# Kernel optimization log

Measured on AMD Instinct MI355X. Metric: run time of the kernel, lower is better.

The kernel has to match this reference:

```python
import jax, jax.numpy as jnp
import numpy as np

B = 32768
NUM_DENSE = 13
PAD_DENSE = 16  # 13 padded up to multiple of 8
T = 26          # number of categorical tables
V = 100000      # cardinality per table
E = 128         # embedding_dim
BOTTOM_DIMS = [512, 256, 128]
TOP_DIMS = [1024, 1024, 512, 256, 1]
N_FEAT = T + 1  # 27 feature vectors entering interaction
PAIR = N_FEAT * (N_FEAT - 1) // 2  # 351
TOP_IN = PAIR + E   # 479
TOP_PAD = 480       # padded to multiple of 8


def _glorot(key, fan_in, fan_out):
    s = np.sqrt(2.0 / (fan_in + fan_out))
    return jax.random.normal(key, (fan_in, fan_out), jnp.float32) * s


def setup_inputs() -> dict:
    key = jax.random.key(0)
    ks = jax.random.split(key, 32)
    inp = {
        "numerical": jax.random.normal(ks[0], (B, NUM_DENSE), jnp.float32),
        "cat_features": jax.random.randint(ks[1], (B, T), 0, V, jnp.int32),
        "emb_tables": jax.random.normal(ks[2], (T, V, E), jnp.float32) * 0.01,
    }
    # bottom MLP: 16 -> 512 -> 256 -> 128 (all relu)
    d_in = PAD_DENSE
    for i, d in enumerate(BOTTOM_DIMS):
        inp[f"bw{i}"] = _glorot(ks[3 + 2 * i], d_in, d)
        inp[f"bb{i}"] = jax.random.normal(ks[4 + 2 * i], (d,), jnp.float32) * np.sqrt(1.0 / d)
        d_in = d
    # top MLP: 480 -> 1024 -> 1024 -> 512 -> 256 -> 1 (relu except last)
    d_in = TOP_PAD
    for i, d in enumerate(TOP_DIMS):
        inp[f"tw{i}"] = _glorot(ks[12 + 2 * i], d_in, d)
        inp[f"tb{i}"] = jax.random.normal(ks[13 + 2 * i], (d,), jnp.float32) * np.sqrt(1.0 / d)
        d_in = d
    return inp


def reference(numerical, cat_features, emb_tables,
              bw0, bb0, bw1, bb1, bw2, bb2,
              tw0, tb0, tw1, tb1, tw2, tb2, tw3, tb3, tw4, tb4):
    b = numerical.shape[0]
    # --- bottom MLP (dense features padded with zeros to 16) ---
    x = jnp.pad(numerical, ((0, 0), (0, PAD_DENSE - NUM_DENSE)))
    for w, bias in ((bw0, bb0), (bw1, bb1), (bw2, bb2)):
        x = jax.nn.relu(x @ w + bias)
    bottom_out = x  # [B, E]
    # --- multi-table embedding gather: emb_tables[t][cat[:, t]] ---
    emb_out = jax.vmap(lambda tab, idx: tab[idx], in_axes=(0, 1), out_axes=1)(
        emb_tables, cat_features)  # [B, T, E]
    # --- dot interaction ---
    feats = jnp.concatenate([bottom_out[:, None, :], emb_out], axis=1)  # [B, 27, E]
    Z = jnp.einsum('bnd,bmd->bnm', feats, feats)  # [B, 27, 27]
    iu, ju = jnp.triu_indices(N_FEAT, k=1)
    pair = Z[:, iu, ju]  # [B, 351]
    x = jnp.concatenate(
        [bottom_out, pair, jnp.zeros((b, TOP_PAD - TOP_IN), feats.dtype)], axis=1)  # [B, 480]
    # --- top MLP (relu except last layer) ---
    tops = ((tw0, tb0), (tw1, tb1), (tw2, tb2), (tw3, tb3), (tw4, tb4))
    for i, (w, bias) in enumerate(tops):
        x = x @ w + bias
        if i < len(tops) - 1:
            x = jax.nn.relu(x)
    return x  # [B, 1] logits
```

## Files before the change

### kernel.cpp

```cpp
#include <hip/hip_runtime.h>

typedef __bf16 bf16;
typedef __bf16 bf16x4 __attribute__((ext_vector_type(4)));
typedef __bf16 bf16x8 __attribute__((ext_vector_type(8)));
typedef float f32x4 __attribute__((ext_vector_type(4)));

#define B_SZ 32768
#define T_CAT 26
#define V_SZ 100000
#define E_SZ 128

__device__ __forceinline__ void gload_lds16(const void* g, void* l) {
    __builtin_amdgcn_global_load_lds(
        (const __attribute__((address_space(1))) void*)g,
        (__attribute__((address_space(3))) void*)l, 16, 0, 0);
}

struct CJob { const float* W; bf16* Wt; int K, N, Kp, blk0; };
struct CJobs { CJob j[7]; };

__global__ __launch_bounds__(256) void convw_all(CJobs js) {
    const int b = blockIdx.x;
    int ji = 0;
#pragma unroll
    for (int k = 1; k < 7; ++k)
        if (b >= js.j[k].blk0) ji = k;
    const CJob J = js.j[ji];
    const int idx = (b - J.blk0) * 256 + threadIdx.x;
    if (idx >= J.Kp * J.N) return;
    const int k = idx / J.N;
    const int n = idx - k * J.N;
    const float v = (k < J.K) ? J.W[(long)k * J.N + n] : 0.0f;
    J.Wt[(long)n * J.Kp + k] = (bf16)v;
}

__global__ __launch_bounds__(256) void make_xpad(const float* __restrict__ num,
                                                 bf16* __restrict__ xp) {
    const int idx = blockIdx.x * 256 + threadIdx.x;
    const int b = idx >> 6, c = idx & 63;
    xp[idx] = (bf16)((c < 13) ? num[(long)b * 13 + c] : 0.0f);
}

template <int RELU>
__global__ __launch_bounds__(256) void gemm_bt(const bf16* __restrict__ A,
                                               const bf16* __restrict__ Bt,
                                               const float* __restrict__ bias,
                                               bf16* __restrict__ C,
                                               int M, int N, int K) {
    __shared__ __align__(16) bf16 As[128 * 64];
    __shared__ __align__(16) bf16 Bs[128 * 64];
    const int t = threadIdx.x;
    const int lane = t & 63;
    const int w = t >> 6;
    const int wm = w >> 1, wn = w & 1;
    const long row0 = (long)blockIdx.y * 128;
    const long col0 = (long)blockIdx.x * 128;

    const int srow = t >> 3;
    const int scol = (t & 7) * 8;
    const bf16* Ag = A + (row0 + srow) * (long)K + scol;
    const bf16* Bg = Bt + (col0 + srow) * (long)K + scol;
    bf16* AsB = &As[w * 512];
    bf16* BsB = &Bs[w * 512];

    f32x4 acc[4][4] = {};

    for (int k0 = 0; k0 < K; k0 += 64) {
#pragma unroll
        for (int q = 0; q < 4; ++q) {
            gload_lds16(Ag + (long)q * 32 * K + k0, AsB + q * 2048);
            gload_lds16(Bg + (long)q * 32 * K + k0, BsB + q * 2048);
        }
        __syncthreads();
#pragma unroll
        for (int s = 0; s < 2; ++s) {
            bf16x8 af[4], bv[4];
#pragma unroll
            for (int i = 0; i < 4; ++i)
                af[i] = *(const bf16x8*)&As[(wm * 64 + i * 16 + (lane & 15)) * 64 +
                                            s * 32 + (lane >> 4) * 8];
#pragma unroll
            for (int j = 0; j < 4; ++j)
                bv[j] = *(const bf16x8*)&Bs[(wn * 64 + j * 16 + (lane & 15)) * 64 +
                                            s * 32 + (lane >> 4) * 8];
#pragma unroll
            for (int i = 0; i < 4; ++i)
#pragma unroll
                for (int j = 0; j < 4; ++j)
                    acc[i][j] = __builtin_amdgcn_mfma_f32_16x16x32_bf16(
                        af[i], bv[j], acc[i][j], 0, 0, 0);
        }
        __syncthreads();
    }

    const int r4 = (lane >> 4) * 4;
    const int cn = lane & 15;
#pragma unroll
    for (int j = 0; j < 4; ++j) {
        const long col = col0 + wn * 64 + j * 16 + cn;
        const float bj = bias[col];
#pragma unroll
        for (int i = 0; i < 4; ++i) {
#pragma unroll
            for (int r = 0; r < 4; ++r) {
                const long row = row0 + wm * 64 + i * 16 + r4 + r;
                float v = acc[i][j][r] + bj;
                if (RELU) v = v > 0.0f ? v : 0.0f;
                C[row * (long)N + col] = (bf16)v;
            }
        }
    }
}

template <int RELU>
__global__ __launch_bounds__(512, 2) void gemm256(const bf16* __restrict__ A,
                                                  const bf16* __restrict__ Bt,
                                                  const float* __restrict__ bias,
                                                  bf16* __restrict__ C,
                                                  int M, int N, int K, int nbx) {
    __shared__ __align__(16) bf16 lds[4 * 2 * 8192];
    const int t = threadIdx.x;
    const int lane = t & 63;
    const int w = t >> 6;
    const int wm = w >> 2, wn = w & 3;

    const int nwg = gridDim.x;
    const int qch = nwg >> 3;
    const int swz = ((int)blockIdx.x & 7) * qch + ((int)blockIdx.x >> 3);
    const int bx = swz % nbx, by = swz / nbx;
    const long row0 = (long)by * 256;
    const long col0 = (long)bx * 256;

    const int NT = K >> 5;

    const int lr = lane >> 2;
    const int dslot = lane & 3;
    const int lrow0 = (w * 2 + 0) * 16 + lr;
    const int lrow1 = (w * 2 + 1) * 16 + lr;
    const int sl0 = dslot ^ ((lrow0 >> 1) & 3);
    const int sl1 = dslot ^ ((lrow1 >> 1) & 3);
    const bf16* Ag0 = A + (row0 + lrow0) * (long)K + sl0 * 8;
    const bf16* Ag1 = A + (row0 + lrow1) * (long)K + sl1 * 8;
    const bf16* Bg0 = Bt + (col0 + lrow0) * (long)K + sl0 * 8;
    const bf16* Bg1 = Bt + (col0 + lrow1) * (long)K + sl1 * 8;
    const int ldsRow0 = (w * 2 + 0) * 512;
    const int ldsRow1 = (w * 2 + 1) * 512;

#define STAGE_A(buf, kt)                                                   \
    do {                                                                   \
        const int _k0 = (kt) << 5;                                         \
        gload_lds16(Ag0 + _k0, &lds[((buf) * 2 + 0) * 8192 + ldsRow0]);    \
        gload_lds16(Ag1 + _k0, &lds[((buf) * 2 + 0) * 8192 + ldsRow1]);    \
    } while (0)
#define STAGE_B(buf, kt)                                                   \
    do {                                                                   \
        const int _k0 = (kt) << 5;                                         \
        gload_lds16(Bg0 + _k0, &lds[((buf) * 2 + 1) * 8192 + ldsRow0]);    \
        gload_lds16(Bg1 + _k0, &lds[((buf) * 2 + 1) * 8192 + ldsRow1]);    \
    } while (0)

    const int cm = lane & 15;
    const int kc = lane >> 4;
    int aoff[8], boff[4];
#pragma unroll
    for (int i = 0; i < 8; ++i) {
        const int r = wm * 128 + i * 16 + cm;
        aoff[i] = r * 32 + (kc ^ ((r >> 1) & 3)) * 8;
    }
#pragma unroll
    for (int j = 0; j < 4; ++j) {
        const int n = wn * 64 + j * 16 + cm;
        boff[j] = n * 32 + (kc ^ ((n >> 1) & 3)) * 8;
    }

    f32x4 acc[8][4] = {};

    STAGE_A(0, 0); STAGE_B(0, 0);
    STAGE_A(1, 1); STAGE_B(1, 1);
    STAGE_A(2, 2); STAGE_B(2, 2);

    for (int tt = 0; tt < NT; ++tt) {
        const int rem = NT - 1 - tt;
        const int sb = (tt + 3) & 3;
        const int sk = tt + 3;

        if (rem >= 2)      asm volatile("s_waitcnt vmcnt(8)" ::: "memory");
        else if (rem == 1) asm volatile("s_waitcnt vmcnt(4)" ::: "memory");
        else               asm volatile("s_waitcnt vmcnt(0)" ::: "memory");
        __builtin_amdgcn_s_barrier();

        const bf16* Ab = &lds[((tt & 3) * 2 + 0) * 8192];
        const bf16* Bb = &lds[((tt & 3) * 2 + 1) * 8192];

        bf16x8 bfr[4], af[4];
#pragma unroll
        for (int j = 0; j < 4; ++j) bfr[j] = *(const bf16x8*)&Bb[boff[j]];
#pragma unroll
        for (int i = 0; i < 4; ++i) af[i] = *(const bf16x8*)&Ab[aoff[i]];
        if (rem >= 3) STAGE_A(sb, sk);
        __builtin_amdgcn_s_barrier();
        __builtin_amdgcn_s_setprio(1);
#pragma unroll
        for (int i = 0; i < 4; ++i)
#pragma unroll
            for (int j = 0; j < 4; ++j)
                acc[i][j] = __builtin_amdgcn_mfma_f32_16x16x32_bf16(
                    af[i], bfr[j], acc[i][j], 0, 0, 0);
        __builtin_amdgcn_s_setprio(0);

        bf16x8 af2[4];
#pragma unroll
        for (int i = 0; i < 4; ++i) af2[i] = *(const bf16x8*)&Ab[aoff[4 + i]];
        if (rem >= 3) STAGE_B(sb, sk);
        __builtin_amdgcn_s_barrier();
        __builtin_amdgcn_s_setprio(1);
#pragma unroll
        for (int i = 0; i < 4; ++i)
#pragma unroll
            for (int j = 0; j < 4; ++j)
                acc[4 + i][j] = __builtin_amdgcn_mfma_f32_16x16x32_bf16(
                    af2[i], bfr[j], acc[4 + i][j], 0, 0, 0);
        __builtin_amdgcn_s_setprio(0);
    }
#undef STAGE_A
#undef STAGE_B

    const int r4 = kc * 4;
#pragma unroll
    for (int j = 0; j < 4; ++j) {
        const long col = col0 + wn * 64 + j * 16 + cm;
        const float bj = bias[col];
#pragma unroll
        for (int i = 0; i < 8; ++i) {
#pragma unroll
            for (int r = 0; r < 4; ++r) {
                const long row = row0 + wm * 128 + i * 16 + r4 + r;
                float v = acc[i][j][r] + bj;
                if (RELU) v = v > 0.0f ? v : 0.0f;
                C[row * (long)N + col] = (bf16)v;
            }
        }
    }
}

__global__ __launch_bounds__(256) void interact_k(const float* __restrict__ emb,
                                                  const int* __restrict__ cat,
                                                  const bf16* __restrict__ bottom,
                                                  bf16* __restrict__ top_in) {
    __shared__ __align__(16) bf16 feats[4][32 * 128];
    __shared__ float gram[4][32 * 32];
    __shared__ __align__(16) bf16 rowbuf[4][512];
    const int t = threadIdx.x;
    const int lane = t & 63;
    const int w = t >> 6;
    const long s = (long)blockIdx.x * 4 + w;

    if (lane < 16)
        ((bf16x8*)&feats[w][0])[lane] = ((const bf16x8*)(bottom + s * 128))[lane];

    const int half = lane >> 5;
    const int le = lane & 31;
#pragma unroll
    for (int it = 0; it < 13; ++it) {
        const int r = 1 + it * 2 + half;
        const int tab = r - 1;
        const int idx = cat[s * T_CAT + tab];
        const float4 v =
            *(const float4*)(emb + ((long)tab * V_SZ + idx) * E_SZ + le * 4);
        bf16x4 o;
        o[0] = (bf16)v.x; o[1] = (bf16)v.y; o[2] = (bf16)v.z; o[3] = (bf16)v.w;
        *(bf16x4*)&feats[w][r * 128 + le * 4] = o;
    }
    __syncthreads();

    bf16x8 f[2][4];
#pragma unroll
    for (int i = 0; i < 2; ++i)
#pragma unroll
        for (int ks = 0; ks < 4; ++ks)
            f[i][ks] = *(const bf16x8*)&feats[w][(i * 16 + (lane & 15)) * 128 +
                                                 ks * 32 + (lane >> 4) * 8];

    f32x4 a00 = {}, a01 = {}, a11 = {};
#pragma unroll
    for (int ks = 0; ks < 4; ++ks) {
        a00 = __builtin_amdgcn_mfma_f32_16x16x32_bf16(f[0][ks], f[0][ks], a00, 0, 0, 0);
        a01 = __builtin_amdgcn_mfma_f32_16x16x32_bf16(f[0][ks], f[1][ks], a01, 0, 0, 0);
        a11 = __builtin_amdgcn_mfma_f32_16x16x32_bf16(f[1][ks], f[1][ks], a11, 0, 0, 0);
    }

    const int r4 = (lane >> 4) * 4;
    const int cn = lane & 15;
#pragma unroll
    for (int r = 0; r < 4; ++r) {
        gram[w][(r4 + r) * 32 + cn]           = a00[r];
        gram[w][(r4 + r) * 32 + 16 + cn]      = a01[r];
        gram[w][(16 + r4 + r) * 32 + 16 + cn] = a11[r];
    }
    __syncthreads();

    if (lane < 16)
        ((bf16x8*)&rowbuf[w][0])[lane] = ((const bf16x8*)&feats[w][0])[lane];
    for (int p = lane; p < 351; p += 64) {
        int i = 0, b = 0;
        while (b + (26 - i) <= p) { b += 26 - i; ++i; }
        const int j = p - b + i + 1;
        rowbuf[w][128 + p] = (bf16)gram[w][i * 32 + j];
    }
    if (lane >= 31) rowbuf[w][448 + lane] = (bf16)0.0f;
    __syncthreads();

    *(bf16x8*)(top_in + s * 512 + lane * 8) = *(const bf16x8*)&rowbuf[w][lane * 8];
}

__global__ __launch_bounds__(256) void gemv_final(const bf16* __restrict__ A,
                                                  const float* __restrict__ w4,
                                                  const float* __restrict__ b4,
                                                  float* __restrict__ out) {
    const int t = threadIdx.x;
    const int lane = t & 63;
    const int w = t >> 6;
    const long m = (long)blockIdx.x * 4 + w;
    const bf16x4 v = *(const bf16x4*)(A + m * 256 + lane * 4);
    const float4 wv = *(const float4*)(w4 + lane * 4);
    float sum = (float)v[0] * wv.x + (float)v[1] * wv.y + (float)v[2] * wv.z +
                (float)v[3] * wv.w;
#pragma unroll
    for (int off = 32; off > 0; off >>= 1) sum += __shfl_down(sum, off);
    if (lane == 0) out[m] = sum + b4[0];
}

extern "C" void kernel_launch(void* const* d_in, const int* in_sizes, int n_in,
                              void* d_out, int out_size, void* d_ws, size_t ws_size,
                              hipStream_t stream) {
    const float* numerical = (const float*)d_in[0];
    const int*   cat       = (const int*)d_in[1];
    const float* emb       = (const float*)d_in[2];
    const float* bw0 = (const float*)d_in[3];
    const float* bb0 = (const float*)d_in[4];
    const float* bw1 = (const float*)d_in[5];
    const float* bb1 = (const float*)d_in[6];
    const float* bw2 = (const float*)d_in[7];
    const float* bb2 = (const float*)d_in[8];
    const float* tw0 = (const float*)d_in[9];
    const float* tb0 = (const float*)d_in[10];
    const float* tw1 = (const float*)d_in[11];
    const float* tb1 = (const float*)d_in[12];
    const float* tw2 = (const float*)d_in[13];
    const float* tb2 = (const float*)d_in[14];
    const float* tw3 = (const float*)d_in[15];
    const float* tb3 = (const float*)d_in[16];
    const float* tw4 = (const float*)d_in[17];
    const float* tb4 = (const float*)d_in[18];
    float* out = (float*)d_out;

    char* ws = (char*)d_ws;
    size_t off = 0;
    auto alloc = [&](size_t bytes) {
        char* p = ws + off;
        off += (bytes + 255) & ~(size_t)255;
        return p;
    };
    bf16* wt0b = (bf16*)alloc((size_t)512 * 64 * 2);
    bf16* wt1b = (bf16*)alloc((size_t)256 * 512 * 2);
    bf16* wt2b = (bf16*)alloc((size_t)128 * 256 * 2);
    bf16* wt0t = (bf16*)alloc((size_t)1024 * 512 * 2);
    bf16* wt1t = (bf16*)alloc((size_t)1024 * 1024 * 2);
    bf16* wt2t = (bf16*)alloc((size_t)512 * 1024 * 2);
    bf16* wt3t = (bf16*)alloc((size_t)256 * 512 * 2);
    bf16* xpad = (bf16*)alloc((size_t)B_SZ * 64 * 2);
    bf16* h0   = (bf16*)alloc((size_t)B_SZ * 512 * 2);
    bf16* h1   = (bf16*)alloc((size_t)B_SZ * 256 * 2);
    bf16* bot  = (bf16*)alloc((size_t)B_SZ * 128 * 2);
    bf16* t0   = (bf16*)alloc((size_t)B_SZ * 1024 * 2);
    bf16* t1   = (bf16*)alloc((size_t)B_SZ * 1024 * 2);
    bf16* top_in = h0;
    bf16* t2 = t0;
    bf16* t3 = t1;

    CJobs js;
    js.j[0] = {bw0, wt0b, 16, 512, 64, 0};
    js.j[1] = {bw1, wt1b, 512, 256, 512, 128};
    js.j[2] = {bw2, wt2b, 256, 128, 256, 640};
    js.j[3] = {tw0, wt0t, 480, 1024, 512, 768};
    js.j[4] = {tw1, wt1t, 1024, 1024, 1024, 2816};
    js.j[5] = {tw2, wt2t, 1024, 512, 1024, 6912};
    js.j[6] = {tw3, wt3t, 512, 256, 512, 8960};
    convw_all<<<9472, 256, 0, stream>>>(js);

    make_xpad<<<(B_SZ * 64) / 256, 256, 0, stream>>>(numerical, xpad);

    gemm_bt<1><<<dim3(4, 256), 256, 0, stream>>>(xpad, wt0b, bb0, h0, B_SZ, 512, 64);
    gemm_bt<1><<<dim3(2, 256), 256, 0, stream>>>(h0, wt1b, bb1, h1, B_SZ, 256, 512);
    gemm_bt<1><<<dim3(1, 256), 256, 0, stream>>>(h1, wt2b, bb2, bot, B_SZ, 128, 256);

    interact_k<<<B_SZ / 4, 256, 0, stream>>>(emb, cat, bot, top_in);

    gemm256<1><<<dim3(4 * 128), 512, 0, stream>>>(top_in, wt0t, tb0, t0, B_SZ, 1024, 512, 4);
    gemm256<1><<<dim3(4 * 128), 512, 0, stream>>>(t0, wt1t, tb1, t1, B_SZ, 1024, 1024, 4);
    gemm256<1><<<dim3(2 * 128), 512, 0, stream>>>(t1, wt2t, tb2, t2, B_SZ, 512, 1024, 2);
    gemm_bt<1><<<dim3(2, 256), 256, 0, stream>>>(t2, wt3t, tb3, t3, B_SZ, 256, 512);

    gemv_final<<<B_SZ / 4, 256, 0, stream>>>(t3, tw4, tb4, out);
}
```

Before: 394.6 us.

## Tile weight transpose, load interaction features straight into registers, switch GEMMs to gemm256

The weight-conversion kernel now transposes through a 64x64 shared-memory tile, so both its reads and its writes are coalesced, and it runs far fewer blocks. The interaction kernel drops its shared feature staging and loads embedding rows directly into MFMA operand registers. It also replaces block-wide __syncthreads with per-wave LDS waits, since each wave only touches its own LDS slice. Two N=256 layers move from gemm_bt to the larger-tile gemm256 kernel, which gives fewer workgroups and may lower occupancy.

```diff
diff --git a/kernel.cpp b/kernel.cpp
--- a/kernel.cpp
+++ b/kernel.cpp
@@ -16,22 +16,40 @@
         (__attribute__((address_space(3))) void*)l, 16, 0, 0);
 }
 
-struct CJob { const float* W; bf16* Wt; int K, N, Kp, blk0; };
+struct CJob { const float* W; bf16* Wt; int K, N, Kp, blk0, tk; };
 struct CJobs { CJob j[7]; };
 
 __global__ __launch_bounds__(256) void convw_all(CJobs js) {
+    __shared__ bf16 tile[64][66];
     const int b = blockIdx.x;
     int ji = 0;
 #pragma unroll
     for (int k = 1; k < 7; ++k)
         if (b >= js.j[k].blk0) ji = k;
     const CJob J = js.j[ji];
-    const int idx = (b - J.blk0) * 256 + threadIdx.x;
-    if (idx >= J.Kp * J.N) return;
-    const int k = idx / J.N;
-    const int n = idx - k * J.N;
-    const float v = (k < J.K) ? J.W[(long)k * J.N + n] : 0.0f;
-    J.Wt[(long)n * J.Kp + k] = (bf16)v;
+    const int local = b - J.blk0;
+    const int tn = local / J.tk;
+    const int tkk = local - tn * J.tk;
+
+    const int t = threadIdx.x;
+    const int lx = t & 63;
+    const int gy = t >> 6;
+
+#pragma unroll
+    for (int kk = 0; kk < 16; ++kk) {
+        const int k = tkk * 64 + kk * 4 + gy;
+        const int n = tn * 64 + lx;
+        const float v = (k < J.K) ? J.W[(long)k * J.N + n] : 0.0f;
+        tile[lx][kk * 4 + gy] = (bf16)v;
+    }
+    __syncthreads();
+#pragma unroll
+    for (int nn = 0; nn < 16; ++nn) {
+        const int nloc = nn * 4 + gy;
+        const int n = tn * 64 + nloc;
+        const int k = tkk * 64 + lx;
+        J.Wt[(long)n * J.Kp + k] = tile[nloc][lx];
+    }
 }
 
 __global__ __launch_bounds__(256) void make_xpad(const float* __restrict__ num,
@@ -247,7 +265,6 @@
                                                   const int* __restrict__ cat,
                                                   const bf16* __restrict__ bottom,
                                                   bf16* __restrict__ top_in) {
-    __shared__ __align__(16) bf16 feats[4][32 * 128];
     __shared__ float gram[4][32 * 32];
     __shared__ __align__(16) bf16 rowbuf[4][512];
     const int t = threadIdx.x;
@@ -255,31 +272,33 @@
     const int w = t >> 6;
     const long s = (long)blockIdx.x * 4 + w;
 
-    if (lane < 16)
-        ((bf16x8*)&feats[w][0])[lane] = ((const bf16x8*)(bottom + s * 128))[lane];
-
-    const int half = lane >> 5;
-    const int le = lane & 31;
-#pragma unroll
-    for (int it = 0; it < 13; ++it) {
-        const int r = 1 + it * 2 + half;
-        const int tab = r - 1;
-        const int idx = cat[s * T_CAT + tab];
-        const float4 v =
-            *(const float4*)(emb + ((long)tab * V_SZ + idx) * E_SZ + le * 4);
-        bf16x4 o;
-        o[0] = (bf16)v.x; o[1] = (bf16)v.y; o[2] = (bf16)v.z; o[3] = (bf16)v.w;
-        *(bf16x4*)&feats[w][r * 128 + le * 4] = o;
-    }
-    __syncthreads();
+    const int rl = lane & 15;
+    const int kg = lane >> 4;
 
     bf16x8 f[2][4];
 #pragma unroll
-    for (int i = 0; i < 2; ++i)
-#pragma unroll
-        for (int ks = 0; ks < 4; ++ks)
-            f[i][ks] = *(const bf16x8*)&feats[w][(i * 16 + (lane & 15)) * 128 +
-                                                 ks * 32 + (lane >> 4) * 8];
+    for (int i = 0; i < 2; ++i) {
+        const int r = i * 16 + rl;
+        const float* rowp = nullptr;
+        if (r >= 1 && r <= 26) {
+            const int idx = cat[s * T_CAT + (r - 1)];
+            rowp = emb + ((long)(r - 1) * V_SZ + idx) * E_SZ;
+        }
+#pragma unroll
+        for (int ks = 0; ks < 4; ++ks) {
+            const int c = ks * 32 + kg * 8;
+            bf16x8 v = {};
+            if (r == 0) {
+                v = *(const bf16x8*)(bottom + s * 128 + c);
+            } else if (r <= 26) {
+                const float4 v0 = *(const float4*)(rowp + c);
+                const float4 v1 = *(const float4*)(rowp + c + 4);
+                v[0]=(bf16)v0.x; v[1]=(bf16)v0.y; v[2]=(bf16)v0.z; v[3]=(bf16)v0.w;
+                v[4]=(bf16)v1.x; v[5]=(bf16)v1.y; v[6]=(bf16)v1.z; v[7]=(bf16)v1.w;
+            }
+            f[i][ks] = v;
+        }
+    }
 
     f32x4 a00 = {}, a01 = {}, a11 = {};
 #pragma unroll
@@ -289,18 +308,18 @@
         a11 = __builtin_amdgcn_mfma_f32_16x16x32_bf16(f[1][ks], f[1][ks], a11, 0, 0, 0);
     }
 
-    const int r4 = (lane >> 4) * 4;
-    const int cn = lane & 15;
+    const int r4 = kg * 4;
 #pragma unroll
     for (int r = 0; r < 4; ++r) {
-        gram[w][(r4 + r) * 32 + cn]           = a00[r];
-        gram[w][(r4 + r) * 32 + 16 + cn]      = a01[r];
-        gram[w][(16 + r4 + r) * 32 + 16 + cn] = a11[r];
-    }
-    __syncthreads();
+        gram[w][(r4 + r) * 32 + rl]           = a00[r];
+        gram[w][(r4 + r) * 32 + 16 + rl]      = a01[r];
+        gram[w][(16 + r4 + r) * 32 + 16 + rl] = a11[r];
+    }
+    asm volatile("s_waitcnt lgkmcnt(0)" ::: "memory");
+    __builtin_amdgcn_sched_barrier(0);
 
     if (lane < 16)
-        ((bf16x8*)&rowbuf[w][0])[lane] = ((const bf16x8*)&feats[w][0])[lane];
+        ((bf16x8*)&rowbuf[w][0])[lane] = ((const bf16x8*)(bottom + s * 128))[lane];
     for (int p = lane; p < 351; p += 64) {
         int i = 0, b = 0;
         while (b + (26 - i) <= p) { b += 26 - i; ++i; }
@@ -308,7 +327,8 @@
         rowbuf[w][128 + p] = (bf16)gram[w][i * 32 + j];
     }
     if (lane >= 31) rowbuf[w][448 + lane] = (bf16)0.0f;
-    __syncthreads();
+    asm volatile("s_waitcnt lgkmcnt(0)" ::: "memory");
+    __builtin_amdgcn_sched_barrier(0);
 
     *(bf16x8*)(top_in + s * 512 + lane * 8) = *(const bf16x8*)&rowbuf[w][lane * 8];
 }
@@ -379,19 +399,19 @@
     bf16* t3 = t1;
 
     CJobs js;
-    js.j[0] = {bw0, wt0b, 16, 512, 64, 0};
-    js.j[1] = {bw1, wt1b, 512, 256, 512, 128};
-    js.j[2] = {bw2, wt2b, 256, 128, 256, 640};
-    js.j[3] = {tw0, wt0t, 480, 1024, 512, 768};
-    js.j[4] = {tw1, wt1t, 1024, 1024, 1024, 2816};
-    js.j[5] = {tw2, wt2t, 1024, 512, 1024, 6912};
-    js.j[6] = {tw3, wt3t, 512, 256, 512, 8960};
-    convw_all<<<9472, 256, 0, stream>>>(js);
+    js.j[0] = {bw0, wt0b, 16, 512, 64, 0, 1};
+    js.j[1] = {bw1, wt1b, 512, 256, 512, 8, 8};
+    js.j[2] = {bw2, wt2b, 256, 128, 256, 40, 4};
+    js.j[3] = {tw0, wt0t, 480, 1024, 512, 48, 8};
+    js.j[4] = {tw1, wt1t, 1024, 1024, 1024, 176, 16};
+    js.j[5] = {tw2, wt2t, 1024, 512, 1024, 432, 16};
+    js.j[6] = {tw3, wt3t, 512, 256, 512, 560, 8};
+    convw_all<<<592, 256, 0, stream>>>(js);
 
     make_xpad<<<(B_SZ * 64) / 256, 256, 0, stream>>>(numerical, xpad);
 
     gemm_bt<1><<<dim3(4, 256), 256, 0, stream>>>(xpad, wt0b, bb0, h0, B_SZ, 512, 64);
-    gemm_bt<1><<<dim3(2, 256), 256, 0, stream>>>(h0, wt1b, bb1, h1, B_SZ, 256, 512);
+    gemm256<1><<<dim3(128), 512, 0, stream>>>(h0, wt1b, bb1, h1, B_SZ, 256, 512, 1);
     gemm_bt<1><<<dim3(1, 256), 256, 0, stream>>>(h1, wt2b, bb2, bot, B_SZ, 128, 256);
 
     interact_k<<<B_SZ / 4, 256, 0, stream>>>(emb, cat, bot, top_in);
@@ -399,7 +419,7 @@
     gemm256<1><<<dim3(4 * 128), 512, 0, stream>>>(top_in, wt0t, tb0, t0, B_SZ, 1024, 512, 4);
     gemm256<1><<<dim3(4 * 128), 512, 0, stream>>>(t0, wt1t, tb1, t1, B_SZ, 1024, 1024, 4);
     gemm256<1><<<dim3(2 * 128), 512, 0, stream>>>(t1, wt2t, tb2, t2, B_SZ, 512, 1024, 2);
-    gemm_bt<1><<<dim3(2, 256), 256, 0, stream>>>(t2, wt3t, tb3, t3, B_SZ, 256, 512);
+    gemm256<1><<<dim3(128), 512, 0, stream>>>(t2, wt3t, tb3, t3, B_SZ, 256, 512, 1);
 
     gemv_final<<<B_SZ / 4, 256, 0, stream>>>(t3, tw4, tb4, out);
 }
```

New measurement: 392.9 us. Within noise of the previous version (-0.4%).
